# Kernel optimization log

Hardware: AMD Instinct MI355X
Metric: run time of the kernel (lower is better)

The kernel has to match this reference:

```python
import jax, jax.numpy as jnp
import numpy as np

D_MODEL = 256
N_HEAD = 8
HEAD_DIM = D_MODEL // N_HEAD
N_TOTAL = 24576
B, T = 64, 512


def setup_inputs() -> dict:
    key = jax.random.key(0)
    ks = jax.random.split(key, 12)
    s = 1.0 / np.sqrt(D_MODEL)
    return {
        "x": jax.random.normal(ks[0], (N_TOTAL, D_MODEL), jnp.float32),
        "Wq": jax.random.uniform(ks[1], (D_MODEL, D_MODEL), jnp.float32, -s, s),
        "bq": jax.random.uniform(ks[2], (D_MODEL,), jnp.float32, -s, s),
        "Wk": jax.random.uniform(ks[3], (D_MODEL, D_MODEL), jnp.float32, -s, s),
        "bk": jax.random.uniform(ks[4], (D_MODEL,), jnp.float32, -s, s),
        "Wv": jax.random.uniform(ks[5], (D_MODEL, D_MODEL), jnp.float32, -s, s),
        "bv": jax.random.uniform(ks[6], (D_MODEL,), jnp.float32, -s, s),
        "Wp": jax.random.uniform(ks[7], (D_MODEL, D_MODEL), jnp.float32, -s, s),
        "bp": jax.random.uniform(ks[8], (D_MODEL,), jnp.float32, -s, s),
        "padpack_index": jax.random.randint(ks[9], (B, T), 0, N_TOTAL, jnp.int64 if jax.config.jax_enable_x64 else jnp.int32),
        "padpack_batch": jax.random.randint(ks[10], (B, T), 0, B, jnp.int32),
        "padpack_inverse_index": jax.random.randint(ks[11], (N_TOTAL,), 0, B * T, jnp.int64 if jax.config.jax_enable_x64 else jnp.int32),
    }


def reference(x, Wq, bq, Wk, bk, Wv, bv, Wp, bp, padpack_index, padpack_batch, padpack_inverse_index):
    # gather ragged tokens into packed [B, T, C]
    xp = x[padpack_index]
    # mask: True where packed slots share the same segment id (matches
    # original masked_fill(batch_i == batch_j, -1e9))
    mask = padpack_batch[:, :, None] == padpack_batch[:, None, :]  # [B,T,T]
    # QKV projections (torch Linear: x @ W.T + b), split heads
    def heads(w, b):
        h = xp @ w.T + b
        return h.reshape(B, T, N_HEAD, HEAD_DIM).transpose(0, 2, 1, 3)  # [B,H,T,D]
    q, k, v = heads(Wq, bq), heads(Wk, bk), heads(Wv, bv)
    att = jnp.einsum("bhtd,bhsd->bhts", q, k) * (1.0 / np.sqrt(HEAD_DIM))
    att = jnp.where(mask[:, None], jnp.float32(-1e9), att)
    att = jax.nn.softmax(att, axis=-1)
    y = jnp.einsum("bhts,bhsd->bhtd", att, v)  # [B,H,T,D]
    y = y.transpose(0, 2, 1, 3).reshape(B, T, D_MODEL)
    y = y @ Wp.T + bp
    # scatter back to ragged layout
    return y.reshape(B * T, D_MODEL)[padpack_inverse_index]
```

## Files before the change

### kernel.cpp

```cpp
#include <hip/hip_runtime.h>


typedef __attribute__((ext_vector_type(8))) short short8;
typedef __attribute__((ext_vector_type(4))) float f32x4;

#define N_TOTAL 24576
#define B_ 64
#define T_ 512
#define DM 256
#define NH 8
#define HD 32
#define F3 768

#define QSCALE 0.25503463f
#define VSP 530

__device__ __forceinline__ unsigned short f2bf(float f) {
  unsigned int u = __float_as_uint(f);
  u += 0x7fffu + ((u >> 16) & 1u);
  return (unsigned short)(u >> 16);
}

__device__ __forceinline__ void gl_lds16(const void* g, void* l) {
  __builtin_amdgcn_global_load_lds(
      (const __attribute__((address_space(1))) unsigned int*)g,
      (__attribute__((address_space(3))) unsigned int*)l, 16, 0, 0);
}

__global__ __launch_bounds__(256) void pack_kernel(
    const float* __restrict__ Wq, const float* __restrict__ Wk,
    const float* __restrict__ Wv, const float* __restrict__ Wp,
    const float* __restrict__ bq, const float* __restrict__ bk,
    const float* __restrict__ bv,
    short* __restrict__ WCAT, short* __restrict__ WPb,
    float* __restrict__ BCAT) {
  int gid = blockIdx.x * 256 + threadIdx.x;
  if (gid < 768)
    BCAT[gid] = (gid < 256) ? bq[gid] : (gid < 512 ? bk[gid - 256] : bv[gid - 512]);
  const float* src;
  short* dst;
  if (gid < 24576) {
    int f = gid >> 5, seg = gid & 31;
    const float* W = (f < 256) ? Wq : ((f < 512) ? Wk : Wv);
    src = W + (size_t)(f & 255) * DM + seg * 8;
    dst = WCAT + (size_t)gid * 8;
  } else {
    int u = gid - 24576;
    src = Wp + (size_t)u * 8;
    dst = WPb + (size_t)u * 8;
  }
  const float4* s4 = (const float4*)src;
  float4 a = s4[0], b = s4[1];
  short8 o;
  o[0] = (short)f2bf(a.x); o[1] = (short)f2bf(a.y);
  o[2] = (short)f2bf(a.z); o[3] = (short)f2bf(a.w);
  o[4] = (short)f2bf(b.x); o[5] = (short)f2bf(b.y);
  o[6] = (short)f2bf(b.z); o[7] = (short)f2bf(b.w);
  *(short8*)dst = o;
}

__global__ __launch_bounds__(256) void qkv_gemm(
    const float* __restrict__ x, const int* __restrict__ idx,
    const short* __restrict__ WCAT, const float* __restrict__ BCAT,
    unsigned short* __restrict__ QKVp) {
  __shared__ __align__(16) char smem[3 * 16384];
  int tid = threadIdx.x;
  int lane = tid & 63, w = tid >> 6;
  int i = lane & 15, q = lane >> 4;
  int m0 = blockIdx.x * 128, n0 = blockIdx.y * 128;
  int wm = (w & 1) * 64, wn = (w >> 1) * 64;
  int csa = q ^ ((i >> 1) & 3);

  int row0 = tid >> 2, c = tid & 3;
  int row1 = 64 + row0;
  int cs0 = c ^ ((row0 >> 1) & 3);
  int cs1 = c ^ ((row1 >> 1) & 3);
  const float* ax0 = x + (size_t)idx[m0 + row0] * DM;
  const float* ax1 = x + (size_t)idx[m0 + row1] * DM;

  f32x4 zf = {0.f, 0.f, 0.f, 0.f};
  f32x4 acc[4][4];
#pragma unroll
  for (int mt = 0; mt < 4; mt++)
#pragma unroll
    for (int nt = 0; nt < 4; nt++) acc[mt][nt] = zf;

  float4 fa[2][2][2];

  auto issueA = [&](int k, int par) {
    fa[par][0][0] = *(const float4*)(ax0 + k * 32 + cs0 * 8);
    fa[par][0][1] = *(const float4*)(ax0 + k * 32 + cs0 * 8 + 4);
    fa[par][1][0] = *(const float4*)(ax1 + k * 32 + cs1 * 8);
    fa[par][1][1] = *(const float4*)(ax1 + k * 32 + cs1 * 8 + 4);
  };
  auto issueB = [&](int k, int s) {
    gl_lds16(WCAT + (size_t)(n0 + row0) * DM + k * 32 + cs0 * 8,
             smem + s * 16384 + 8192 + tid * 16);
    gl_lds16(WCAT + (size_t)(n0 + row1) * DM + k * 32 + cs1 * 8,
             smem + s * 16384 + 8192 + (256 + tid) * 16);
  };
  auto writeA = [&](int s, int par) {
    short8 o0, o1;
    float4 l0 = fa[par][0][0], h0 = fa[par][0][1];
    float4 l1 = fa[par][1][0], h1 = fa[par][1][1];
    o0[0] = (short)f2bf(l0.x); o0[1] = (short)f2bf(l0.y);
    o0[2] = (short)f2bf(l0.z); o0[3] = (short)f2bf(l0.w);
    o0[4] = (short)f2bf(h0.x); o0[5] = (short)f2bf(h0.y);
    o0[6] = (short)f2bf(h0.z); o0[7] = (short)f2bf(h0.w);
    o1[0] = (short)f2bf(l1.x); o1[1] = (short)f2bf(l1.y);
    o1[2] = (short)f2bf(l1.z); o1[3] = (short)f2bf(l1.w);
    o1[4] = (short)f2bf(h1.x); o1[5] = (short)f2bf(h1.y);
    o1[6] = (short)f2bf(h1.z); o1[7] = (short)f2bf(h1.w);
    *(short8*)(smem + s * 16384 + tid * 16) = o0;
    *(short8*)(smem + s * 16384 + (256 + tid) * 16) = o1;
  };

  issueA(0, 0);
  issueB(0, 0);
  issueA(1, 1);
  issueB(1, 1);
  asm volatile("s_waitcnt vmcnt(8)" ::: "memory");
  writeA(0, 0);

#pragma unroll
  for (int k = 0; k < 8; k++) {
    if (k == 7)
      asm volatile("s_waitcnt vmcnt(0) lgkmcnt(0)\ns_barrier" ::: "memory");
    else
      asm volatile("s_waitcnt vmcnt(6) lgkmcnt(0)\ns_barrier" ::: "memory");
    const short* Asb = (const short*)(smem + (k % 3) * 16384);
    const short* Bsb = Asb + 4096;
    short8 a[4], bfr[4];
#pragma unroll
    for (int mt = 0; mt < 4; mt++)
      a[mt] = *(const short8*)&Asb[(wm + mt * 16 + i) * 32 + csa * 8];
#pragma unroll
    for (int nt = 0; nt < 4; nt++)
      bfr[nt] = *(const short8*)&Bsb[(wn + nt * 16 + i) * 32 + csa * 8];
    if (k < 6) {
      issueA(k + 2, k & 1);
      issueB(k + 2, (k + 2) % 3);
    }
#pragma unroll
    for (int mt = 0; mt < 4; mt++)
#pragma unroll
      for (int nt = 0; nt < 4; nt++)
        acc[mt][nt] = __builtin_amdgcn_mfma_f32_16x16x32_bf16(a[mt], bfr[nt], acc[mt][nt], 0, 0, 0);
    if (k < 7) {
      if (k < 6)
        asm volatile("s_waitcnt vmcnt(8)" ::: "memory");
      else
        asm volatile("s_waitcnt vmcnt(2)" ::: "memory");
      writeA((k + 1) % 3, (k + 1) & 1);
    }
  }

  float scale = (n0 < 256) ? QSCALE : 1.0f;
#pragma unroll
  for (int nt = 0; nt < 4; nt++) {
    int f = n0 + wn + nt * 16 + i;
    float bias = BCAT[f];
#pragma unroll
    for (int mt = 0; mt < 4; mt++) {
#pragma unroll
      for (int r = 0; r < 4; r++) {
        int token = m0 + wm + mt * 16 + q * 4 + r;
        QKVp[(size_t)token * F3 + f] = f2bf((acc[mt][nt][r] + bias) * scale);
      }
    }
  }
}

__global__ __launch_bounds__(512, 4) void attn_kernel(
    const unsigned short* __restrict__ QKVp, const int* __restrict__ batch,
    unsigned short* __restrict__ Y) {
  __shared__ __align__(16) short Vl[HD * VSP];
  __shared__ int sbat[T_];
  int tid = threadIdx.x, w = tid >> 6, lane = tid & 63;
  int i = lane & 15, q = lane >> 4;
  int bx = blockIdx.x;
  int h = bx >> 6, b = bx & 63;
  int t0 = w * 64;
  const unsigned short* Tok = QKVp + (size_t)b * T_ * F3;

  sbat[tid] = batch[b * T_ + tid];

  {
    int seg = tid & 3, sb = tid >> 2;
#pragma unroll
    for (int l = 0; l < 4; l++) {
      int s = sb + l * 128;
      short8 v = *(const short8*)&Tok[(size_t)s * F3 + 512 + h * HD + seg * 8];
#pragma unroll
      for (int j = 0; j < 8; j++) Vl[(seg * 8 + j) * VSP + s] = v[j];
    }
  }
  __syncthreads();

  short8 qf[4];
  int btm[4];
#pragma unroll
  for (int mt = 0; mt < 4; mt++)
    qf[mt] = *(const short8*)&Tok[(size_t)(t0 + mt * 16 + i) * F3 + h * HD + q * 8];
#pragma unroll
  for (int mt = 0; mt < 4; mt++) btm[mt] = sbat[t0 + mt * 16 + i];

  unsigned short ob = (i == 0) ? (unsigned short)0x3F80 : (unsigned short)0;
  short8 ones = {(short)ob, (short)ob, (short)ob, (short)ob,
                 (short)ob, (short)ob, (short)ob, (short)ob};

  f32x4 zf = {0.f, 0.f, 0.f, 0.f};
  f32x4 o[4][2], lacc[4];
#pragma unroll
  for (int mt = 0; mt < 4; mt++) {
    o[mt][0] = zf; o[mt][1] = zf; lacc[mt] = zf;
  }

  const unsigned short* Kb = Tok + 256 + h * HD + q * 8;
  short8 k0f = *(const short8*)&Kb[(size_t)(i)*F3];
  short8 k1f = *(const short8*)&Kb[(size_t)(16 + i) * F3];

  for (int s0 = 0; s0 < T_; s0 += 32) {
    short8 ck0 = k0f, ck1 = k1f;
    if (s0 + 32 < T_) {
      k0f = *(const short8*)&Kb[(size_t)(s0 + 32 + i) * F3];
      k1f = *(const short8*)&Kb[(size_t)(s0 + 48 + i) * F3];
    }
    int4 bs0 = *(const int4*)&sbat[s0 + q * 4];
    int4 bs1 = *(const int4*)&sbat[s0 + 16 + q * 4];
    short8 v0f = *(const short8*)&Vl[i * VSP + s0 + q * 8];
    short8 v1f = *(const short8*)&Vl[(16 + i) * VSP + s0 + q * 8];
#pragma unroll
    for (int mt = 0; mt < 4; mt++) {
      f32x4 st0 = __builtin_amdgcn_mfma_f32_16x16x32_bf16(ck0, qf[mt], zf, 0, 0, 0);
      f32x4 st1 = __builtin_amdgcn_mfma_f32_16x16x32_bf16(ck1, qf[mt], zf, 0, 0, 0);
      int bm = btm[mt];
      float e00 = __builtin_amdgcn_exp2f((bs0.x == bm) ? -1e9f : st0[0]);
      float e01 = __builtin_amdgcn_exp2f((bs0.y == bm) ? -1e9f : st0[1]);
      float e02 = __builtin_amdgcn_exp2f((bs0.z == bm) ? -1e9f : st0[2]);
      float e03 = __builtin_amdgcn_exp2f((bs0.w == bm) ? -1e9f : st0[3]);
      float e10 = __builtin_amdgcn_exp2f((bs1.x == bm) ? -1e9f : st1[0]);
      float e11 = __builtin_amdgcn_exp2f((bs1.y == bm) ? -1e9f : st1[1]);
      float e12 = __builtin_amdgcn_exp2f((bs1.z == bm) ? -1e9f : st1[2]);
      float e13 = __builtin_amdgcn_exp2f((bs1.w == bm) ? -1e9f : st1[3]);
      unsigned A0 = __builtin_amdgcn_perm(__float_as_uint(e01), __float_as_uint(e00), 0x07060302u);
      unsigned A1 = __builtin_amdgcn_perm(__float_as_uint(e03), __float_as_uint(e02), 0x07060302u);
      unsigned B0 = __builtin_amdgcn_perm(__float_as_uint(e11), __float_as_uint(e10), 0x07060302u);
      unsigned B1 = __builtin_amdgcn_perm(__float_as_uint(e13), __float_as_uint(e12), 0x07060302u);
      asm volatile(
          "s_nop 1\n\t"
          "v_permlane32_swap_b32 %0, %2\n\t"
          "v_permlane32_swap_b32 %1, %3\n\t"
          "s_nop 1\n\t"
          "v_permlane16_swap_b32 %0, %2\n\t"
          "v_permlane16_swap_b32 %1, %3\n\t"
          "s_nop 1"
          : "+v"(A0), "+v"(A1), "+v"(B0), "+v"(B1));
      union {
        unsigned u[4];
        short8 s;
      } cv;
      cv.u[0] = A0;
      cv.u[1] = A1;
      cv.u[2] = B0;
      cv.u[3] = B1;
      short8 pa = cv.s;
      o[mt][0] = __builtin_amdgcn_mfma_f32_16x16x32_bf16(pa, v0f, o[mt][0], 0, 0, 0);
      o[mt][1] = __builtin_amdgcn_mfma_f32_16x16x32_bf16(pa, v1f, o[mt][1], 0, 0, 0);
      lacc[mt] = __builtin_amdgcn_mfma_f32_16x16x32_bf16(pa, ones, lacc[mt], 0, 0, 0);
    }
  }

#pragma unroll
  for (int mt = 0; mt < 4; mt++) {
#pragma unroll
    for (int r = 0; r < 4; r++) {
      float lv = __shfl(lacc[mt][r], lane & 48, 64);
      float inv = __builtin_amdgcn_rcpf(lv);
      size_t yb = ((size_t)b * T_ + t0 + mt * 16 + q * 4 + r) * DM + h * HD;
      Y[yb + i] = f2bf(o[mt][0][r] * inv);
      Y[yb + 16 + i] = f2bf(o[mt][1][r] * inv);
    }
  }
}

__global__ __launch_bounds__(256) void out_gemm(
    const short* __restrict__ Y, const short* __restrict__ WPb,
    const float* __restrict__ bp, const int* __restrict__ inv,
    float* __restrict__ out) {
  __shared__ __align__(16) char smem[3 * 16384];
  int tid = threadIdx.x;
  int lane = tid & 63, w = tid >> 6;
  int i = lane & 15, q = lane >> 4;
  int m0 = blockIdx.x * 128, n0 = blockIdx.y * 128;
  int wm = (w & 1) * 64, wn = (w >> 1) * 64;
  int csa = q ^ ((i >> 1) & 3);

  int iv0 = inv[m0 + (tid >> 2)];
  int iv1 = inv[m0 + 64 + (tid >> 2)];

  f32x4 zf = {0.f, 0.f, 0.f, 0.f};
  f32x4 acc[4][4];
#pragma unroll
  for (int mt = 0; mt < 4; mt++)
#pragma unroll
    for (int nt = 0; nt < 4; nt++) acc[mt][nt] = zf;

  auto stage = [&](int k, int s) {
#pragma unroll
    for (int p = 0; p < 2; p++) {
      int U = p * 256 + tid;
      int row = U >> 2, c = U & 3;
      int cs = c ^ ((row >> 1) & 3);
      int iv = p ? iv1 : iv0;
      gl_lds16(Y + (size_t)iv * DM + k * 32 + cs * 8, smem + s * 16384 + U * 16);
      gl_lds16(WPb + (size_t)(n0 + row) * DM + k * 32 + cs * 8,
               smem + s * 16384 + 8192 + U * 16);
    }
  };

  stage(0, 0);
  stage(1, 1);
#pragma unroll
  for (int k = 0; k < 8; k++) {
    if (k == 7)
      asm volatile("s_waitcnt vmcnt(0) lgkmcnt(0)\ns_barrier" ::: "memory");
    else
      asm volatile("s_waitcnt vmcnt(4) lgkmcnt(0)\ns_barrier" ::: "memory");
    const short* Asb = (const short*)(smem + (k % 3) * 16384);
    const short* Bsb = Asb + 4096;
    short8 a[4], bfr[4];
#pragma unroll
    for (int mt = 0; mt < 4; mt++)
      a[mt] = *(const short8*)&Asb[(wm + mt * 16 + i) * 32 + csa * 8];
#pragma unroll
    for (int nt = 0; nt < 4; nt++)
      bfr[nt] = *(const short8*)&Bsb[(wn + nt * 16 + i) * 32 + csa * 8];
    if (k < 6) stage(k + 2, (k + 2) % 3);
#pragma unroll
    for (int mt = 0; mt < 4; mt++)
#pragma unroll
      for (int nt = 0; nt < 4; nt++)
        acc[mt][nt] = __builtin_amdgcn_mfma_f32_16x16x32_bf16(a[mt], bfr[nt], acc[mt][nt], 0, 0, 0);
  }

#pragma unroll
  for (int nt = 0; nt < 4; nt++) {
    int f = n0 + wn + nt * 16 + i;
    float bias = bp[f];
#pragma unroll
    for (int mt = 0; mt < 4; mt++) {
#pragma unroll
      for (int r = 0; r < 4; r++) {
        int row = m0 + wm + mt * 16 + q * 4 + r;
        out[(size_t)row * DM + f] = acc[mt][nt][r] + bias;
      }
    }
  }
}

extern "C" void kernel_launch(void* const* d_in, const int* in_sizes, int n_in,
                              void* d_out, int out_size, void* d_ws, size_t ws_size,
                              hipStream_t stream) {
  const float* x = (const float*)d_in[0];
  const float* Wq = (const float*)d_in[1];
  const float* bq = (const float*)d_in[2];
  const float* Wk = (const float*)d_in[3];
  const float* bk = (const float*)d_in[4];
  const float* Wv = (const float*)d_in[5];
  const float* bv = (const float*)d_in[6];
  const float* Wp = (const float*)d_in[7];
  const float* bp = (const float*)d_in[8];
  const int* idx = (const int*)d_in[9];
  const int* batch = (const int*)d_in[10];
  const int* inv = (const int*)d_in[11];
  float* out = (float*)d_out;

  char* ws = (char*)d_ws;
  short* WCAT = (short*)(ws + 0);
  short* WPb = (short*)(ws + 524288);
  float* BCAT = (float*)(ws + 1048576);
  unsigned short* QKVp = (unsigned short*)(ws + 2097152);
  unsigned short* Yb = (unsigned short*)(ws + 52428800);

  pack_kernel<<<128, 256, 0, stream>>>(Wq, Wk, Wv, Wp, bq, bk, bv,
                                       WCAT, WPb, BCAT);
  qkv_gemm<<<dim3(256, 6), 256, 0, stream>>>(x, idx, WCAT, BCAT, QKVp);
  attn_kernel<<<512, 512, 0, stream>>>(QKVp, batch, Yb);
  out_gemm<<<dim3(192, 2), 256, 0, stream>>>((const short*)Yb, WPb, bp, inv, out);
}
```

Measured before the change: 163.9 us.

## Keep gathered A tile resident in LDS and loop over all QKV output panels

The QKV GEMM now has each block own 64 gathered tokens. It converts their full 256-wide rows to bf16 once into LDS, then sweeps all six 128-column weight panels, streaming B through a triple buffer. Before, the 128x128 tiling re-gathered and re-converted the same x rows for each of the 6 column blocks. This removes that redundant gather and conversion traffic. In exchange, each block does less MFMA work per barrier, uses more LDS, and launches 512 blocks instead of 1536, which may reduce latency hiding.

```diff
diff --git a/kernel.cpp b/kernel.cpp
--- a/kernel.cpp
+++ b/kernel.cpp
@@ -63,109 +63,92 @@
     const float* __restrict__ x, const int* __restrict__ idx,
     const short* __restrict__ WCAT, const float* __restrict__ BCAT,
     unsigned short* __restrict__ QKVp) {
-  __shared__ __align__(16) char smem[3 * 16384];
+  __shared__ __align__(16) char Asm[8 * 4096];
+  __shared__ __align__(16) char Bsm[3 * 8192];
   int tid = threadIdx.x;
   int lane = tid & 63, w = tid >> 6;
   int i = lane & 15, q = lane >> 4;
-  int m0 = blockIdx.x * 128, n0 = blockIdx.y * 128;
-  int wm = (w & 1) * 64, wn = (w >> 1) * 64;
+  int m0 = blockIdx.x * 64;
+  int wn = w * 32;
   int csa = q ^ ((i >> 1) & 3);
 
-  int row0 = tid >> 2, c = tid & 3;
-  int row1 = 64 + row0;
-  int cs0 = c ^ ((row0 >> 1) & 3);
-  int cs1 = c ^ ((row1 >> 1) & 3);
-  const float* ax0 = x + (size_t)idx[m0 + row0] * DM;
-  const float* ax1 = x + (size_t)idx[m0 + row1] * DM;
+  int row = tid >> 2, c = tid & 3;
+  int cs0 = c ^ ((row >> 1) & 3);
+  int brow1 = 64 + row;
+  int cs1 = c ^ ((brow1 >> 1) & 3);
+  const float* ax = x + (size_t)idx[m0 + row] * DM;
+
+  auto issueB = [&](int g, int s) {
+    int p = g >> 3, k = g & 7;
+    gl_lds16(WCAT + (size_t)(p * 128 + row) * DM + k * 32 + cs0 * 8,
+             Bsm + s * 8192 + tid * 16);
+    gl_lds16(WCAT + (size_t)(p * 128 + brow1) * DM + k * 32 + cs1 * 8,
+             Bsm + s * 8192 + (256 + tid) * 16);
+  };
+
+  issueB(0, 0);
+  issueB(1, 1);
+#pragma unroll
+  for (int k = 0; k < 8; k++) {
+    float4 lo = *(const float4*)(ax + k * 32 + cs0 * 8);
+    float4 hi = *(const float4*)(ax + k * 32 + cs0 * 8 + 4);
+    short8 o;
+    o[0] = (short)f2bf(lo.x); o[1] = (short)f2bf(lo.y);
+    o[2] = (short)f2bf(lo.z); o[3] = (short)f2bf(lo.w);
+    o[4] = (short)f2bf(hi.x); o[5] = (short)f2bf(hi.y);
+    o[6] = (short)f2bf(hi.z); o[7] = (short)f2bf(hi.w);
+    *(short8*)(Asm + k * 4096 + tid * 16) = o;
+  }
+  asm volatile("s_waitcnt vmcnt(2) lgkmcnt(0)\ns_barrier" ::: "memory");
 
   f32x4 zf = {0.f, 0.f, 0.f, 0.f};
-  f32x4 acc[4][4];
-#pragma unroll
-  for (int mt = 0; mt < 4; mt++)
-#pragma unroll
-    for (int nt = 0; nt < 4; nt++) acc[mt][nt] = zf;
-
-  float4 fa[2][2][2];
-
-  auto issueA = [&](int k, int par) {
-    fa[par][0][0] = *(const float4*)(ax0 + k * 32 + cs0 * 8);
-    fa[par][0][1] = *(const float4*)(ax0 + k * 32 + cs0 * 8 + 4);
-    fa[par][1][0] = *(const float4*)(ax1 + k * 32 + cs1 * 8);
-    fa[par][1][1] = *(const float4*)(ax1 + k * 32 + cs1 * 8 + 4);
-  };
-  auto issueB = [&](int k, int s) {
-    gl_lds16(WCAT + (size_t)(n0 + row0) * DM + k * 32 + cs0 * 8,
-             smem + s * 16384 + 8192 + tid * 16);
-    gl_lds16(WCAT + (size_t)(n0 + row1) * DM + k * 32 + cs1 * 8,
-             smem + s * 16384 + 8192 + (256 + tid) * 16);
-  };
-  auto writeA = [&](int s, int par) {
-    short8 o0, o1;
-    float4 l0 = fa[par][0][0], h0 = fa[par][0][1];
-    float4 l1 = fa[par][1][0], h1 = fa[par][1][1];
-    o0[0] = (short)f2bf(l0.x); o0[1] = (short)f2bf(l0.y);
-    o0[2] = (short)f2bf(l0.z); o0[3] = (short)f2bf(l0.w);
-    o0[4] = (short)f2bf(h0.x); o0[5] = (short)f2bf(h0.y);
-    o0[6] = (short)f2bf(h0.z); o0[7] = (short)f2bf(h0.w);
-    o1[0] = (short)f2bf(l1.x); o1[1] = (short)f2bf(l1.y);
-    o1[2] = (short)f2bf(l1.z); o1[3] = (short)f2bf(l1.w);
-    o1[4] = (short)f2bf(h1.x); o1[5] = (short)f2bf(h1.y);
-    o1[6] = (short)f2bf(h1.z); o1[7] = (short)f2bf(h1.w);
-    *(short8*)(smem + s * 16384 + tid * 16) = o0;
-    *(short8*)(smem + s * 16384 + (256 + tid) * 16) = o1;
-  };
-
-  issueA(0, 0);
-  issueB(0, 0);
-  issueA(1, 1);
-  issueB(1, 1);
-  asm volatile("s_waitcnt vmcnt(8)" ::: "memory");
-  writeA(0, 0);
-
-#pragma unroll
-  for (int k = 0; k < 8; k++) {
-    if (k == 7)
-      asm volatile("s_waitcnt vmcnt(0) lgkmcnt(0)\ns_barrier" ::: "memory");
-    else
-      asm volatile("s_waitcnt vmcnt(6) lgkmcnt(0)\ns_barrier" ::: "memory");
-    const short* Asb = (const short*)(smem + (k % 3) * 16384);
-    const short* Bsb = Asb + 4096;
-    short8 a[4], bfr[4];
-#pragma unroll
-    for (int mt = 0; mt < 4; mt++)
-      a[mt] = *(const short8*)&Asb[(wm + mt * 16 + i) * 32 + csa * 8];
-#pragma unroll
-    for (int nt = 0; nt < 4; nt++)
-      bfr[nt] = *(const short8*)&Bsb[(wn + nt * 16 + i) * 32 + csa * 8];
-    if (k < 6) {
-      issueA(k + 2, k & 1);
-      issueB(k + 2, (k + 2) % 3);
-    }
-#pragma unroll
-    for (int mt = 0; mt < 4; mt++)
-#pragma unroll
-      for (int nt = 0; nt < 4; nt++)
-        acc[mt][nt] = __builtin_amdgcn_mfma_f32_16x16x32_bf16(a[mt], bfr[nt], acc[mt][nt], 0, 0, 0);
-    if (k < 7) {
-      if (k < 6)
-        asm volatile("s_waitcnt vmcnt(8)" ::: "memory");
-      else
-        asm volatile("s_waitcnt vmcnt(2)" ::: "memory");
-      writeA((k + 1) % 3, (k + 1) & 1);
-    }
-  }
-
-  float scale = (n0 < 256) ? QSCALE : 1.0f;
-#pragma unroll
-  for (int nt = 0; nt < 4; nt++) {
-    int f = n0 + wn + nt * 16 + i;
-    float bias = BCAT[f];
-#pragma unroll
-    for (int mt = 0; mt < 4; mt++) {
-#pragma unroll
-      for (int r = 0; r < 4; r++) {
-        int token = m0 + wm + mt * 16 + q * 4 + r;
-        QKVp[(size_t)token * F3 + f] = f2bf((acc[mt][nt][r] + bias) * scale);
+  f32x4 acc[4][2];
+#pragma unroll
+  for (int mt = 0; mt < 4; mt++) {
+    acc[mt][0] = zf;
+    acc[mt][1] = zf;
+  }
+
+#pragma unroll 1
+  for (int p = 0; p < 6; p++) {
+#pragma unroll
+    for (int k = 0; k < 8; k++) {
+      int g = p * 8 + k;
+      if (g > 0) {
+        if (g == 47)
+          asm volatile("s_waitcnt vmcnt(0) lgkmcnt(0)\ns_barrier" ::: "memory");
+        else
+          asm volatile("s_waitcnt vmcnt(2) lgkmcnt(0)\ns_barrier" ::: "memory");
+      }
+      const short* Asb = (const short*)(Asm + k * 4096);
+      const short* Bsb = (const short*)(Bsm + (g % 3) * 8192);
+      short8 a[4], bfr[2];
+#pragma unroll
+      for (int mt = 0; mt < 4; mt++)
+        a[mt] = *(const short8*)&Asb[(mt * 16 + i) * 32 + csa * 8];
+#pragma unroll
+      for (int nt = 0; nt < 2; nt++)
+        bfr[nt] = *(const short8*)&Bsb[(wn + nt * 16 + i) * 32 + csa * 8];
+      if (g + 2 < 48) issueB(g + 2, (g + 2) % 3);
+#pragma unroll
+      for (int mt = 0; mt < 4; mt++) {
+        acc[mt][0] = __builtin_amdgcn_mfma_f32_16x16x32_bf16(a[mt], bfr[0], acc[mt][0], 0, 0, 0);
+        acc[mt][1] = __builtin_amdgcn_mfma_f32_16x16x32_bf16(a[mt], bfr[1], acc[mt][1], 0, 0, 0);
+      }
+    }
+    float scale = (p < 2) ? QSCALE : 1.0f;
+#pragma unroll
+    for (int nt = 0; nt < 2; nt++) {
+      int f = p * 128 + wn + nt * 16 + i;
+      float bias = BCAT[f];
+#pragma unroll
+      for (int mt = 0; mt < 4; mt++) {
+#pragma unroll
+        for (int r = 0; r < 4; r++) {
+          int token = m0 + mt * 16 + q * 4 + r;
+          QKVp[(size_t)token * F3 + f] = f2bf((acc[mt][nt][r] + bias) * scale);
+        }
+        acc[mt][nt] = zf;
       }
     }
   }
@@ -385,7 +368,7 @@
 
   pack_kernel<<<128, 256, 0, stream>>>(Wq, Wk, Wv, Wp, bq, bk, bv,
                                        WCAT, WPb, BCAT);
-  qkv_gemm<<<dim3(256, 6), 256, 0, stream>>>(x, idx, WCAT, BCAT, QKVp);
+  qkv_gemm<<<512, 256, 0, stream>>>(x, idx, WCAT, BCAT, QKVp);
   attn_kernel<<<512, 512, 0, stream>>>(QKVp, batch, Yb);
   out_gemm<<<dim3(192, 2), 256, 0, stream>>>((const short*)Yb, WPb, bp, inv, out);
 }
```

New measurement: 163.9 us. Within noise of the previous version (+0.0%).
